# Kernel tuning notes

Hardware: AMD Instinct MI355X
Metric: run time of the kernel (lower is better)

Reference implementation:

```python
import jax, jax.numpy as jnp
import numpy as np

NUM_HEADS = 8
GROUPS = 32
EPS = 1e-5


def setup_inputs() -> dict:
    key = jax.random.key(0)
    k1, k2, k3 = jax.random.split(key, 3)
    B, C, H, W = 16, 512, 64, 64
    x = jax.random.normal(k1, (B, C, H, W), dtype=jnp.float32)
    scale = C ** -0.5  # keep qkv/proj outputs well-scaled
    return {
        "x": x,
        "norm_w": jnp.ones((C,), jnp.float32),
        "norm_b": jnp.zeros((C,), jnp.float32),
        "qkv_w": jax.random.normal(k2, (3 * C, C), dtype=jnp.float32) * scale,
        "qkv_b": jnp.zeros((3 * C,), jnp.float32),
        "proj_w": jax.random.normal(k3, (C, C), dtype=jnp.float32) * scale,
        "proj_b": jnp.zeros((C,), jnp.float32),
    }


def reference(x, norm_w, norm_b, qkv_w, qkv_b, proj_w, proj_b):
    B, C, H, W = x.shape
    N = H * W
    nh = NUM_HEADS
    hd = C // nh

    # GroupNorm(32, C)
    xg = x.reshape(B, GROUPS, C // GROUPS, N)
    mu = xg.mean(axis=(2, 3), keepdims=True)
    var = xg.var(axis=(2, 3), keepdims=True)
    h = ((xg - mu) * jax.lax.rsqrt(var + EPS)).reshape(B, C, N)
    h = h * norm_w[None, :, None] + norm_b[None, :, None]

    h = h.transpose(0, 2, 1)  # [B, N, C]
    qkv = (h @ qkv_w.T + qkv_b).reshape(B, N, 3, nh, hd)
    q, k, v = qkv[:, :, 0], qkv[:, :, 1], qkv[:, :, 2]  # each [B, N, nh, hd]

    # Faithful to source: attention over the HEAD axis at each position
    attn = jnp.einsum('bnhd,bngd->bnhg', q, k) * (hd ** -0.5)  # [B, N, nh, nh]
    attn = jax.nn.softmax(attn, axis=-1)
    o = jnp.einsum('bnhg,bngd->bnhd', attn, v).reshape(B, N, C)

    o = o @ proj_w.T + proj_b  # [B, N, C]
    return x + o.transpose(0, 2, 1).reshape(B, C, H, W)
```

## Files before the change

kernel.cpp:

```cpp
#include <hip/hip_runtime.h>

typedef __attribute__((ext_vector_type(8))) short short8v;
typedef __attribute__((ext_vector_type(4))) float float4v;
typedef unsigned short ushortT;

__device__ __forceinline__ unsigned short f2bf(float f) {
  union { float f; unsigned u; } a; a.f = f;
  unsigned r = a.u + 0x7fffu + ((a.u >> 16) & 1u);
  return (unsigned short)(r >> 16);
}
__device__ __forceinline__ float2 up2(unsigned u) {
  union { unsigned u; float f; } a, b;
  a.u = u << 16; b.u = u & 0xffff0000u;
  return make_float2(a.f, b.f);
}
__device__ __forceinline__ void gl_lds16(const void* g, void* l) {
  __builtin_amdgcn_global_load_lds(
      (const __attribute__((address_space(1))) void*)g,
      (__attribute__((address_space(3))) void*)l, 16, 0, 0);
}

#define WAITV8 asm volatile("s_waitcnt vmcnt(8)" ::: "memory")
#define WAITV4 asm volatile("s_waitcnt vmcnt(4)" ::: "memory")
#define WAITV0 asm volatile("s_waitcnt vmcnt(0)" ::: "memory")
#define BAR()  __builtin_amdgcn_s_barrier()

__global__ __launch_bounds__(256) void wconv(const float* __restrict__ src,
                                             ushortT* __restrict__ dst, int n) {
  int i = (blockIdx.x * 256 + threadIdx.x) * 4;
  if (i < n) {
    float4 v = *(const float4*)(src + i);
    uint2 o;
    o.x = (unsigned)f2bf(v.x) | ((unsigned)f2bf(v.y) << 16);
    o.y = (unsigned)f2bf(v.z) | ((unsigned)f2bf(v.w) << 16);
    *(uint2*)(dst + i) = o;
  }
}

__global__ __launch_bounds__(256) void gn_stats(const float* __restrict__ x,
                                                float2* __restrict__ stats) {
  int bg = blockIdx.x;
  const float* base = x + (size_t)bg * 65536;
  int tid = threadIdx.x;
  float s = 0.f, s2 = 0.f;
  for (int i = tid; i < 16384; i += 256) {
    float4 v = *(const float4*)(base + (size_t)i * 4);
    s  += v.x + v.y + v.z + v.w;
    s2 += v.x * v.x + v.y * v.y + v.z * v.z + v.w * v.w;
  }
  #pragma unroll
  for (int off = 32; off > 0; off >>= 1) {
    s  += __shfl_down(s, off);
    s2 += __shfl_down(s2, off);
  }
  __shared__ float red[8];
  int w = tid >> 6, l = tid & 63;
  if (l == 0) { red[w] = s; red[w + 4] = s2; }
  __syncthreads();
  if (tid == 0) {
    float ts = red[0] + red[1] + red[2] + red[3];
    float t2 = red[4] + red[5] + red[6] + red[7];
    float mean = ts * (1.f / 65536.f);
    float var  = t2 * (1.f / 65536.f) - mean * mean;
    stats[bg] = make_float2(mean, rsqrtf(var + 1e-5f));
  }
}

__global__ __launch_bounds__(512) void norm_tr(const float* __restrict__ x,
                                               const float* __restrict__ nw,
                                               const float* __restrict__ nb,
                                               const float2* __restrict__ stats,
                                               ushortT* __restrict__ h) {
  __shared__ float t[64][65];
  int n0 = blockIdx.x * 64, c0 = blockIdx.y * 64, b = blockIdx.z;
  int tx = threadIdx.x, ty = threadIdx.y;
  #pragma unroll
  for (int j = ty; j < 64; j += 8) {
    int c = c0 + j;
    float2 ms = stats[b * 32 + (c >> 4)];
    float v = x[((size_t)b * 512 + c) * 4096 + n0 + tx];
    t[j][tx] = (v - ms.x) * ms.y * nw[c] + nb[c];
  }
  __syncthreads();
  #pragma unroll
  for (int j = ty; j < 64; j += 8) {
    int n = n0 + j;
    h[((size_t)b * 4096 + n) * 512 + c0 + tx] = f2bf(t[tx][j]);
  }
}

__device__ __forceinline__ void core256(const ushortT* __restrict__ A,
                                        const ushortT* __restrict__ Bm,
                                        ushortT* lds, int m0, int n0,
                                        float4v (&acc)[8][4]) {
  const int tid = threadIdx.x;
  const int w = tid >> 6, l = tid & 63;
  const int wm = w >> 2, wn = w & 3;
  const int ra = w * 32 + (l >> 2);
  const int sc = ((l & 3) ^ ((ra >> 1) & 3)) * 8;
  const ushortT* pa = A + (size_t)(m0 + ra) * 512 + sc;
  const ushortT* pb = Bm + (size_t)(n0 + ra) * 512 + sc;
  const int dstoff = w * 1024;
  const int swz = ((l >> 4) ^ (((l & 15) >> 1) & 3)) * 8;
  const int baseA = (wm * 128 + (l & 15)) * 32 + swz;
  const int baseB = 8192 + (wn * 64 + (l & 15)) * 32 + swz;

  auto stageA = [&](int t) {
    ushortT* d = lds + (t & 3) * 16384 + dstoff;
    gl_lds16(pa + t * 32, d);
    gl_lds16(pa + t * 32 + 16 * 512, d + 512);
  };
  auto stageB = [&](int t) {
    ushortT* d = lds + (t & 3) * 16384 + 8192 + dstoff;
    gl_lds16(pb + t * 32, d);
    gl_lds16(pb + t * 32 + 16 * 512, d + 512);
  };

  stageA(0); stageB(0); stageA(1); stageB(1); stageA(2); stageB(2);
  WAITV8; BAR();

  #pragma unroll 1
  for (int t = 0; t < 16; ++t) {
    const ushortT* buf = lds + (t & 3) * 16384;
    short8v a[8];
    #pragma unroll
    for (int fm = 0; fm < 8; ++fm)
      a[fm] = *(const short8v*)(buf + baseA + fm * 512);
    short8v b0 = *(const short8v*)(buf + baseB);
    short8v b1 = *(const short8v*)(buf + baseB + 512);
    if (t + 3 < 16) stageA(t + 3);
    BAR();
    __builtin_amdgcn_s_setprio(1);
    #pragma unroll
    for (int fm = 0; fm < 8; ++fm) {
      acc[fm][0] = __builtin_amdgcn_mfma_f32_16x16x32_bf16(a[fm], b0, acc[fm][0], 0, 0, 0);
      acc[fm][1] = __builtin_amdgcn_mfma_f32_16x16x32_bf16(a[fm], b1, acc[fm][1], 0, 0, 0);
    }
    __builtin_amdgcn_s_setprio(0);
    BAR();
    short8v b2 = *(const short8v*)(buf + baseB + 1024);
    short8v b3 = *(const short8v*)(buf + baseB + 1536);
    if (t + 3 < 16) stageB(t + 3);
    BAR();
    __builtin_amdgcn_s_setprio(1);
    #pragma unroll
    for (int fm = 0; fm < 8; ++fm) {
      acc[fm][2] = __builtin_amdgcn_mfma_f32_16x16x32_bf16(a[fm], b2, acc[fm][2], 0, 0, 0);
      acc[fm][3] = __builtin_amdgcn_mfma_f32_16x16x32_bf16(a[fm], b3, acc[fm][3], 0, 0, 0);
    }
    __builtin_amdgcn_s_setprio(0);
    if (t <= 12)      { WAITV8; }
    else if (t == 13) { WAITV4; }
    else              { WAITV0; }
    BAR();
  }
}

__global__ __launch_bounds__(512, 2) void gemm_qkv(const ushortT* __restrict__ h,
                                                   const ushortT* __restrict__ wq,
                                                   const float* __restrict__ bias,
                                                   ushortT* __restrict__ outq) {
  __shared__ ushortT lds[65536];
  int bid = blockIdx.x;
  int wg = (bid & 7) * 192 + (bid >> 3);
  int m0 = (wg / 6) * 256, n0 = (wg % 6) * 256;
  float4v acc[8][4] = {};
  core256(h, wq, lds, m0, n0, acc);
  const int tid = threadIdx.x;
  const int w = tid >> 6, l = tid & 63;
  const int wm = w >> 2, wn = w & 3;
  __syncthreads();
  ushortT* es = lds + w * 1280;
  float bb[4];
  #pragma unroll
  for (int fn = 0; fn < 4; ++fn) bb[fn] = bias[n0 + wn * 64 + fn * 16 + (l & 15)];
  int r = l >> 2, g = l & 3;
  #pragma unroll
  for (int fm = 0; fm < 8; ++fm) {
    #pragma unroll
    for (int fn = 0; fn < 4; ++fn)
      #pragma unroll
      for (int j = 0; j < 4; ++j)
        es[((l >> 4) * 4 + j) * 72 + fn * 16 + (l & 15)] = f2bf(acc[fm][fn][j] + bb[fn]);
    uint4 v0 = *(const uint4*)(es + r * 72 + g * 16);
    uint4 v1 = *(const uint4*)(es + r * 72 + g * 16 + 8);
    size_t mrow = (size_t)m0 + wm * 128 + fm * 16 + r;
    uint4* dst = (uint4*)(outq + mrow * 1536 + n0 + wn * 64 + g * 16);
    dst[0] = v0; dst[1] = v1;
  }
}

__global__ __launch_bounds__(256) void attn_k(const ushortT* __restrict__ qkv,
                                              ushortT* __restrict__ o) {
  int gp = blockIdx.x * 256 + threadIdx.x;
  int pos = gp >> 3, hh = gp & 7;
  const ushortT* base = qkv + (size_t)pos * 1536;
  float q[64];
  #pragma unroll
  for (int i = 0; i < 8; ++i) {
    uint4 u = *(const uint4*)(base + hh * 64 + i * 8);
    float2 t0 = up2(u.x), t1 = up2(u.y), t2 = up2(u.z), t3 = up2(u.w);
    q[i*8+0]=t0.x; q[i*8+1]=t0.y; q[i*8+2]=t1.x; q[i*8+3]=t1.y;
    q[i*8+4]=t2.x; q[i*8+5]=t2.y; q[i*8+6]=t3.x; q[i*8+7]=t3.y;
  }
  float lg[8];
  #pragma unroll
  for (int g = 0; g < 8; ++g) {
    float s = 0.f;
    #pragma unroll
    for (int d8 = 0; d8 < 8; ++d8) {
      uint4 kk = *(const uint4*)(base + 512 + g * 64 + d8 * 8);
      float2 k0 = up2(kk.x), k1 = up2(kk.y), k2 = up2(kk.z), k3 = up2(kk.w);
      s += q[d8*8+0]*k0.x + q[d8*8+1]*k0.y + q[d8*8+2]*k1.x + q[d8*8+3]*k1.y
         + q[d8*8+4]*k2.x + q[d8*8+5]*k2.y + q[d8*8+6]*k3.x + q[d8*8+7]*k3.y;
    }
    lg[g] = s * 0.125f;
  }
  float mx = lg[0];
  #pragma unroll
  for (int g = 1; g < 8; ++g) mx = fmaxf(mx, lg[g]);
  float ssum = 0.f;
  #pragma unroll
  for (int g = 0; g < 8; ++g) { lg[g] = __expf(lg[g] - mx); ssum += lg[g]; }
  float inv = 1.f / ssum;
  #pragma unroll
  for (int g = 0; g < 8; ++g) lg[g] *= inv;
  float oa[64];
  #pragma unroll
  for (int i = 0; i < 64; ++i) oa[i] = 0.f;
  #pragma unroll
  for (int g = 0; g < 8; ++g) {
    float wg = lg[g];
    #pragma unroll
    for (int d8 = 0; d8 < 8; ++d8) {
      uint4 vv = *(const uint4*)(base + 1024 + g * 64 + d8 * 8);
      float2 v0 = up2(vv.x), v1 = up2(vv.y), v2 = up2(vv.z), v3 = up2(vv.w);
      oa[d8*8+0] += wg*v0.x; oa[d8*8+1] += wg*v0.y;
      oa[d8*8+2] += wg*v1.x; oa[d8*8+3] += wg*v1.y;
      oa[d8*8+4] += wg*v2.x; oa[d8*8+5] += wg*v2.y;
      oa[d8*8+6] += wg*v3.x; oa[d8*8+7] += wg*v3.y;
    }
  }
  ushortT* dst = o + (size_t)pos * 512 + hh * 64;
  #pragma unroll
  for (int i = 0; i < 8; ++i) {
    uint4 w_;
    w_.x = (unsigned)f2bf(oa[i*8+0]) | ((unsigned)f2bf(oa[i*8+1]) << 16);
    w_.y = (unsigned)f2bf(oa[i*8+2]) | ((unsigned)f2bf(oa[i*8+3]) << 16);
    w_.z = (unsigned)f2bf(oa[i*8+4]) | ((unsigned)f2bf(oa[i*8+5]) << 16);
    w_.w = (unsigned)f2bf(oa[i*8+6]) | ((unsigned)f2bf(oa[i*8+7]) << 16);
    *(uint4*)(dst + i * 8) = w_;
  }
}

__global__ __launch_bounds__(512, 2) void gemm_proj(const ushortT* __restrict__ o,
                                                    const ushortT* __restrict__ wp,
                                                    const float* __restrict__ bias,
                                                    const float* __restrict__ x,
                                                    float* __restrict__ out) {
  __shared__ ushortT lds[65536];
  int bid = blockIdx.x;
  int wg = (bid & 7) * 64 + (bid >> 3);
  int m0 = (wg >> 1) * 256, n0 = (wg & 1) * 256;
  float4v acc[8][4] = {};
  core256(o, wp, lds, m0, n0, acc);
  const int tid = threadIdx.x;
  const int w = tid >> 6, l = tid & 63;
  const int wm = w >> 2, wn = w & 3;
  __syncthreads();
  float* es = (float*)((char*)lds + w * 4608);
  int b = m0 >> 12;
  int c = n0 + wn * 64 + l;
  float bc = bias[c];
  const float* xrow = x + ((size_t)b * 512 + c) * 4096;
  float* orow = out + ((size_t)b * 512 + c) * 4096;
  int nb0 = (m0 & 4095) + wm * 128;
  #pragma unroll
  for (int fm = 0; fm < 8; ++fm) {
    #pragma unroll
    for (int fn = 0; fn < 4; ++fn)
      #pragma unroll
      for (int j = 0; j < 4; ++j)
        es[((l >> 4) * 4 + j) * 68 + fn * 16 + (l & 15)] = acc[fm][fn][j];
    int nb = nb0 + fm * 16;
    #pragma unroll
    for (int q4 = 0; q4 < 4; ++q4) {
      float4 xv = *(const float4*)(xrow + nb + q4 * 4);
      float4 ov;
      ov.x = xv.x + bc + es[(q4 * 4 + 0) * 68 + l];
      ov.y = xv.y + bc + es[(q4 * 4 + 1) * 68 + l];
      ov.z = xv.z + bc + es[(q4 * 4 + 2) * 68 + l];
      ov.w = xv.w + bc + es[(q4 * 4 + 3) * 68 + l];
      *(float4*)(orow + nb + q4 * 4) = ov;
    }
  }
}

extern "C" void kernel_launch(void* const* d_in, const int* in_sizes, int n_in,
                              void* d_out, int out_size, void* d_ws, size_t ws_size,
                              hipStream_t stream) {
  const float* x     = (const float*)d_in[0];
  const float* nw    = (const float*)d_in[1];
  const float* nb    = (const float*)d_in[2];
  const float* qkvw  = (const float*)d_in[3];
  const float* qkvb  = (const float*)d_in[4];
  const float* pw    = (const float*)d_in[5];
  const float* pb    = (const float*)d_in[6];
  float* out = (float*)d_out;
  char* ws = (char*)d_ws;

  const size_t OFF_WQ   = 4096;
  const size_t OFF_WP   = OFF_WQ + 1572864;
  const size_t OFF_H    = OFF_WP + 524288;
  const size_t OFF_QKV  = OFF_H + 67108864;

  float2* stats   = (float2*)ws;
  ushortT* wq_b   = (ushortT*)(ws + OFF_WQ);
  ushortT* wp_b   = (ushortT*)(ws + OFF_WP);
  ushortT* h      = (ushortT*)(ws + OFF_H);
  ushortT* qkv    = (ushortT*)(ws + OFF_QKV);

  wconv<<<768, 256, 0, stream>>>(qkvw, wq_b, 786432);
  wconv<<<256, 256, 0, stream>>>(pw,   wp_b, 262144);
  gn_stats<<<512, 256, 0, stream>>>(x, stats);
  norm_tr<<<dim3(64, 8, 16), dim3(64, 8), 0, stream>>>(x, nw, nb, stats, h);
  gemm_qkv<<<1536, 512, 0, stream>>>(h, wq_b, qkvb, qkv);
  attn_k<<<2048, 256, 0, stream>>>(qkv, h);
  gemm_proj<<<512, 512, 0, stream>>>(h, wp_b, pb, x, out);
}
```

Baseline: 428.0 us.

## Prefetch next K-tile LDS fragments into double-buffered registers during MFMA phases

The GEMM core loop now loads the next tile's A and B fragments from LDS into a second register set, interleaved with the current tile's MFMA phases, using ping-pong register arrays and a loop unrolled by two. Waits are tightened so the next LDS buffer's global loads have completed before those early reads. The aim is to hide LDS read latency behind matrix math. In exchange it roughly doubles the A/B fragment register footprint, which risks spills under the 512-thread, 2-block launch bound, and the changed vmcnt accounting must stay correct.

```diff
diff --git a/kernel.cpp b/kernel.cpp
--- a/kernel.cpp
+++ b/kernel.cpp
@@ -20,10 +20,10 @@
       (__attribute__((address_space(3))) void*)l, 16, 0, 0);
 }
 
-#define WAITV8 asm volatile("s_waitcnt vmcnt(8)" ::: "memory")
 #define WAITV4 asm volatile("s_waitcnt vmcnt(4)" ::: "memory")
 #define WAITV0 asm volatile("s_waitcnt vmcnt(0)" ::: "memory")
 #define BAR()  __builtin_amdgcn_s_barrier()
+#define MFMA16(d, a, b) d = __builtin_amdgcn_mfma_f32_16x16x32_bf16(a, b, d, 0, 0, 0)
 
 __global__ __launch_bounds__(256) void wconv(const float* __restrict__ src,
                                              ushortT* __restrict__ dst, int n) {
@@ -116,43 +116,59 @@
     gl_lds16(pb + t * 32 + 16 * 512, d + 512);
   };
 
+  short8v aX[8], aY[8], b0X, b1X, b0Y, b1Y, bB0, bB1;
+
   stageA(0); stageB(0); stageA(1); stageB(1); stageA(2); stageB(2);
-  WAITV8; BAR();
-
-  #pragma unroll 1
-  for (int t = 0; t < 16; ++t) {
-    const ushortT* buf = lds + (t & 3) * 16384;
-    short8v a[8];
-    #pragma unroll
-    for (int fm = 0; fm < 8; ++fm)
-      a[fm] = *(const short8v*)(buf + baseA + fm * 512);
-    short8v b0 = *(const short8v*)(buf + baseB);
-    short8v b1 = *(const short8v*)(buf + baseB + 512);
+  WAITV4; BAR();
+  #pragma unroll
+  for (int i = 0; i < 8; ++i) aX[i] = *(const short8v*)(lds + baseA + i * 512);
+  b0X = *(const short8v*)(lds + baseB);
+  b1X = *(const short8v*)(lds + baseB + 512);
+
+  auto tile = [&](int t, short8v (&ac)[8], short8v (&an)[8],
+                  short8v& b0c, short8v& b1c, short8v& b0n, short8v& b1n) {
+    const ushortT* buf  = lds + (t & 3) * 16384;
+    const ushortT* bufN = lds + ((t + 1) & 3) * 16384;
+    bB0 = *(const short8v*)(buf + baseB + 1024);
+    bB1 = *(const short8v*)(buf + baseB + 1536);
+    if (t < 15) {
+      #pragma unroll
+      for (int i = 0; i < 4; ++i) an[i] = *(const short8v*)(bufN + baseA + i * 512);
+    }
     if (t + 3 < 16) stageA(t + 3);
     BAR();
     __builtin_amdgcn_s_setprio(1);
     #pragma unroll
     for (int fm = 0; fm < 8; ++fm) {
-      acc[fm][0] = __builtin_amdgcn_mfma_f32_16x16x32_bf16(a[fm], b0, acc[fm][0], 0, 0, 0);
-      acc[fm][1] = __builtin_amdgcn_mfma_f32_16x16x32_bf16(a[fm], b1, acc[fm][1], 0, 0, 0);
+      MFMA16(acc[fm][0], ac[fm], b0c);
+      MFMA16(acc[fm][1], ac[fm], b1c);
     }
     __builtin_amdgcn_s_setprio(0);
     BAR();
-    short8v b2 = *(const short8v*)(buf + baseB + 1024);
-    short8v b3 = *(const short8v*)(buf + baseB + 1536);
+    if (t < 15) {
+      #pragma unroll
+      for (int i = 4; i < 8; ++i) an[i] = *(const short8v*)(bufN + baseA + i * 512);
+      b0n = *(const short8v*)(bufN + baseB);
+      b1n = *(const short8v*)(bufN + baseB + 512);
+    }
     if (t + 3 < 16) stageB(t + 3);
     BAR();
     __builtin_amdgcn_s_setprio(1);
     #pragma unroll
     for (int fm = 0; fm < 8; ++fm) {
-      acc[fm][2] = __builtin_amdgcn_mfma_f32_16x16x32_bf16(a[fm], b2, acc[fm][2], 0, 0, 0);
-      acc[fm][3] = __builtin_amdgcn_mfma_f32_16x16x32_bf16(a[fm], b3, acc[fm][3], 0, 0, 0);
+      MFMA16(acc[fm][2], ac[fm], bB0);
+      MFMA16(acc[fm][3], ac[fm], bB1);
     }
     __builtin_amdgcn_s_setprio(0);
-    if (t <= 12)      { WAITV8; }
-    else if (t == 13) { WAITV4; }
-    else              { WAITV0; }
+    if (t <= 12)      { WAITV4; }
+    else if (t == 13) { WAITV0; }
     BAR();
+  };
+
+  #pragma unroll 1
+  for (int tt = 0; tt < 16; tt += 2) {
+    tile(tt,     aX, aY, b0X, b1X, b0Y, b1Y);
+    tile(tt + 1, aY, aX, b0Y, b1Y, b0X, b1X);
   }
 }
 
```

Measured after the change: 409.2 us. 1.05x faster.

## Restructure GEMM mainloop to K=64 double-buffered tiles with quadrant MFMA clusters

Applied to the files above, without the earlier changes.

Replaces the 4-stage K=32 pipeline in the shared GEMM core with a 2-buffer K=64 scheme. Each K tile is staged as four 128-row half-tiles with an XOR swizzle, and the MFMA work is split into four quadrant clusters, each preceded by fragment reads and interleaved with async global-to-LDS loads for the next tile. The aim is to halve the loop iterations and barrier count per K, and to keep fewer A fragments live at once so register pressure drops. In exchange there are more barriers inside each tile, explicit lgkmcnt waits, and a more fragile ordering of staging writes into the buffer being consumed. The old core256 (also rewritten) is left unused.

```diff
diff --git a/kernel.cpp b/kernel.cpp
--- a/kernel.cpp
+++ b/kernel.cpp
@@ -20,10 +20,11 @@
       (__attribute__((address_space(3))) void*)l, 16, 0, 0);
 }
 
-#define WAITV8 asm volatile("s_waitcnt vmcnt(8)" ::: "memory")
 #define WAITV4 asm volatile("s_waitcnt vmcnt(4)" ::: "memory")
 #define WAITV0 asm volatile("s_waitcnt vmcnt(0)" ::: "memory")
+#define LGKM0  asm volatile("s_waitcnt lgkmcnt(0)" ::: "memory")
 #define BAR()  __builtin_amdgcn_s_barrier()
+#define MFMA16(d, a, b) d = __builtin_amdgcn_mfma_f32_16x16x32_bf16(a, b, d, 0, 0, 0)
 
 __global__ __launch_bounds__(256) void wconv(const float* __restrict__ src,
                                              ushortT* __restrict__ dst, int n) {
@@ -93,67 +94,199 @@
                                         const ushortT* __restrict__ Bm,
                                         ushortT* lds, int m0, int n0,
                                         float4v (&acc)[8][4]) {
+  char* ldsb = (char*)lds;
   const int tid = threadIdx.x;
   const int w = tid >> 6, l = tid & 63;
   const int wm = w >> 2, wn = w & 3;
-  const int ra = w * 32 + (l >> 2);
-  const int sc = ((l & 3) ^ ((ra >> 1) & 3)) * 8;
-  const ushortT* pa = A + (size_t)(m0 + ra) * 512 + sc;
-  const ushortT* pb = Bm + (size_t)(n0 + ra) * 512 + sc;
-  const int dstoff = w * 1024;
-  const int swz = ((l >> 4) ^ (((l & 15) >> 1) & 3)) * 8;
-  const int baseA = (wm * 128 + (l & 15)) * 32 + swz;
-  const int baseB = 8192 + (wn * 64 + (l & 15)) * 32 + swz;
-
-  auto stageA = [&](int t) {
-    ushortT* d = lds + (t & 3) * 16384 + dstoff;
-    gl_lds16(pa + t * 32, d);
-    gl_lds16(pa + t * 32 + 16 * 512, d + 512);
-  };
-  auto stageB = [&](int t) {
-    ushortT* d = lds + (t & 3) * 16384 + 8192 + dstoff;
-    gl_lds16(pb + t * 32, d);
-    gl_lds16(pb + t * 32 + 16 * 512, d + 512);
-  };
-
-  stageA(0); stageB(0); stageA(1); stageB(1); stageA(2); stageB(2);
-  WAITV8; BAR();
+
+  const int P0b = tid * 16, P1b = 8192 + tid * 16;
+  const int r0 = P0b >> 7, r1 = P1b >> 7;
+  const int s0 = (P0b & 127) ^ ((r0 & 7) << 4);
+  const int s1 = (P1b & 127) ^ ((r1 & 7) << 4);
+  const size_t g0 = (size_t)r0 * 512 + (s0 >> 1);
+  const size_t g1 = (size_t)r1 * 512 + (s1 >> 1);
+  auto stage = [&](const ushortT* mat, int rowbase, int kt, int bufb, int region) {
+    const ushortT* gsrc = mat + (size_t)rowbase * 512 + kt * 64;
+    char* dbase = ldsb + bufb + region;
+    gl_lds16(gsrc + g0, dbase + P0b);
+    gl_lds16(gsrc + g1, dbase + P1b);
+  };
+
+  const int colb = (l >> 4) * 16;
+  const int cs0 = colb ^ ((l & 7) << 4);
+  const int cs1 = (64 + colb) ^ ((l & 7) << 4);
+  const int arow = wm * 16384 + (l & 15) * 128;
+  const int brow = 32768 + wn * 8192 + (l & 15) * 128;
+
+  short8v Af[4][2], Bf[4][2];
+  auto rdA = [&](int bb, int m, int mhalf) {
+    const char* p = ldsb + bb + arow + m * 2048;
+    Af[m][0] = *(const short8v*)(p + cs0);
+    Af[m][1] = *(const short8v*)(p + cs1);
+    (void)mhalf;
+  };
+  auto rdB = [&](int bb, int n) {
+    const char* p = ldsb + bb + brow + n * 2048;
+    Bf[n][0] = *(const short8v*)(p + cs0);
+    Bf[n][1] = *(const short8v*)(p + cs1);
+  };
+
+  #define CLUSTER(MH, NP)                                              \
+    { __builtin_amdgcn_s_setprio(1);                                   \
+      _Pragma("unroll")                                                \
+      for (int mm = 0; mm < 4; ++mm) {                                 \
+        _Pragma("unroll")                                              \
+        for (int nn = 0; nn < 2; ++nn) {                               \
+          MFMA16(acc[(MH)*4+mm][(NP)*2+nn], Af[mm][0], Bf[(NP)*2+nn][0]); \
+          MFMA16(acc[(MH)*4+mm][(NP)*2+nn], Af[mm][1], Bf[(NP)*2+nn][1]); \
+        } }                                                            \
+      __builtin_amdgcn_s_setprio(0); }
+
+  auto tile = [&](int bb, int t1, int t2, bool s1g, bool s2g, int vw) {
+    rdA(bb, 0, 0); rdA(bb, 1, 0); rdA(bb, 2, 0); rdA(bb, 3, 0);
+    rdB(bb, 0); rdB(bb, 1);
+    if (s1g) stage(A, m0 + 128, t1, bb ^ 65536, 16384);
+    BAR(); LGKM0;
+    CLUSTER(0, 0);
+    BAR();
+    rdB(bb, 2); rdB(bb, 3);
+    if (s1g) stage(Bm, n0 + 128, t1, bb ^ 65536, 49152);
+    BAR(); LGKM0;
+    CLUSTER(0, 1);
+    BAR();
+    rdA(bb, 0, 1); rdA(bb, 1, 1); rdA(bb, 2, 1); rdA(bb, 3, 1);
+    if (s2g) stage(Bm, n0, t2, bb, 32768);
+    BAR(); LGKM0;
+    CLUSTER(1, 1);
+    BAR();
+    if (s2g) stage(A, m0, t2, bb, 0);
+    if (vw == 4)      { WAITV4; }
+    else if (vw == 0) { WAITV0; }
+    BAR();
+    CLUSTER(1, 0);
+    BAR();
+  };
+  #undef CLUSTER
+
+
+  stage(A,  m0,       0, 0, 0);
+  stage(A,  m0 + 128, 0, 0, 16384);
+  stage(Bm, n0,       0, 0, 32768);
+  stage(Bm, n0 + 128, 0, 0, 49152);
+  stage(Bm, n0,       1, 65536, 32768);
+  stage(A,  m0,       1, 65536, 0);
+  WAITV4;
+  BAR();
 
   #pragma unroll 1
-  for (int t = 0; t < 16; ++t) {
-    const ushortT* buf = lds + (t & 3) * 16384;
-    short8v a[8];
-    #pragma unroll
-    for (int fm = 0; fm < 8; ++fm)
-      a[fm] = *(const short8v*)(buf + baseA + fm * 512);
-    short8v b0 = *(const short8v*)(buf + baseB);
-    short8v b1 = *(const short8v*)(buf + baseB + 512);
-    if (t + 3 < 16) stageA(t + 3);
-    BAR();
-    __builtin_amdgcn_s_setprio(1);
-    #pragma unroll
-    for (int fm = 0; fm < 8; ++fm) {
-      acc[fm][0] = __builtin_amdgcn_mfma_f32_16x16x32_bf16(a[fm], b0, acc[fm][0], 0, 0, 0);
-      acc[fm][1] = __builtin_amdgcn_mfma_f32_16x16x32_bf16(a[fm], b1, acc[fm][1], 0, 0, 0);
-    }
-    __builtin_amdgcn_s_setprio(0);
-    BAR();
-    short8v b2 = *(const short8v*)(buf + baseB + 1024);
-    short8v b3 = *(const short8v*)(buf + baseB + 1536);
-    if (t + 3 < 16) stageB(t + 3);
-    BAR();
-    __builtin_amdgcn_s_setprio(1);
-    #pragma unroll
-    for (int fm = 0; fm < 8; ++fm) {
-      acc[fm][2] = __builtin_amdgcn_mfma_f32_16x16x32_bf16(a[fm], b2, acc[fm][2], 0, 0, 0);
-      acc[fm][3] = __builtin_amdgcn_mfma_f32_16x16x32_bf16(a[fm], b3, acc[fm][3], 0, 0, 0);
-    }
-    __builtin_amdgcn_s_setprio(0);
-    if (t <= 12)      { WAITV8; }
-    else if (t == 13) { WAITV4; }
-    else              { WAITV0; }
-    BAR();
-  }
+  for (int tp = 0; tp < 3; ++tp) {
+    int ta = 2 * tp, tb = 2 * tp + 1;
+    tile(0,     ta + 1, ta + 2, true, true, 4);
+    tile(65536, tb + 1, tb + 2, true, true, 4);
+  }
+  tile(0,     7, 8, true,  false, 0);
+  tile(65536, 8, 9, false, false, -1);
+}
+
+
+__device__ __forceinline__ void core256b(const ushortT* __restrict__ A,
+                                         const ushortT* __restrict__ Bm,
+                                         ushortT* lds, int m0, int n0,
+                                         float4v (&acc)[8][4]) {
+  char* ldsb = (char*)lds;
+  const int tid = threadIdx.x;
+  const int w = tid >> 6, l = tid & 63;
+  const int wm = w >> 2, wn = w & 3;
+
+  const int P0b = tid * 16, P1b = 8192 + tid * 16;
+  const int r0 = P0b >> 7, r1 = P1b >> 7;
+  const int s0 = (P0b & 127) ^ ((r0 & 7) << 4);
+  const int s1 = (P1b & 127) ^ ((r1 & 7) << 4);
+  const size_t g0 = (size_t)r0 * 512 + (s0 >> 1);
+  const size_t g1 = (size_t)r1 * 512 + (s1 >> 1);
+  auto stage = [&](const ushortT* mat, int rowbase, int kt, int bufb, int region) {
+    const ushortT* gsrc = mat + (size_t)rowbase * 512 + kt * 64;
+    char* dbase = ldsb + bufb + region;
+    gl_lds16(gsrc + g0, dbase + P0b);
+    gl_lds16(gsrc + g1, dbase + P1b);
+  };
+
+  const int colb = (l >> 4) * 16;
+  const int cs0 = colb ^ ((l & 7) << 4);
+  const int cs1 = (64 + colb) ^ ((l & 7) << 4);
+  const int arow = wm * 16384 + (l & 15) * 128;
+  const int brow = 32768 + wn * 8192 + (l & 15) * 128;
+
+  short8v Af[4][2], Bf[4][2];
+
+  #define RDA4(bb, MH)                                                  \
+    { _Pragma("unroll")                                                 \
+      for (int mm = 0; mm < 4; ++mm) {                                  \
+        const char* p = ldsb + (bb) + arow + ((MH)*4 + mm) * 2048;      \
+        Af[mm][0] = *(const short8v*)(p + cs0);                         \
+        Af[mm][1] = *(const short8v*)(p + cs1);                         \
+      } }
+  #define RDB2(bb, N0)                                                  \
+    { _Pragma("unroll")                                                 \
+      for (int nn = 0; nn < 2; ++nn) {                                  \
+        const char* p = ldsb + (bb) + brow + ((N0) + nn) * 2048;        \
+        Bf[(N0)+nn][0] = *(const short8v*)(p + cs0);                    \
+        Bf[(N0)+nn][1] = *(const short8v*)(p + cs1);                    \
+      } }
+  #define CLUSTER(MH, NP)                                               \
+    { __builtin_amdgcn_s_setprio(1);                                    \
+      _Pragma("unroll")                                                 \
+      for (int mm = 0; mm < 4; ++mm) {                                  \
+        _Pragma("unroll")                                               \
+        for (int nn = 0; nn < 2; ++nn) {                                \
+          MFMA16(acc[(MH)*4+mm][(NP)*2+nn], Af[mm][0], Bf[(NP)*2+nn][0]); \
+          MFMA16(acc[(MH)*4+mm][(NP)*2+nn], Af[mm][1], Bf[(NP)*2+nn][1]); \
+        } }                                                             \
+      __builtin_amdgcn_s_setprio(0); }
+
+  auto tile = [&](int bb, int t1, int t2, bool s1g, bool s2g, int vw) {
+    RDA4(bb, 0); RDB2(bb, 0);
+    if (s1g) stage(A, m0 + 128, t1, bb ^ 65536, 16384);
+    BAR(); LGKM0;
+    CLUSTER(0, 0);
+    BAR();
+    RDB2(bb, 2);
+    if (s1g) stage(Bm, n0 + 128, t1, bb ^ 65536, 49152);
+    BAR(); LGKM0;
+    CLUSTER(0, 1);
+    BAR();
+    RDA4(bb, 1);
+    if (s2g) stage(Bm, n0, t2, bb, 32768);
+    BAR(); LGKM0;
+    CLUSTER(1, 1);
+    BAR();
+    if (s2g) stage(A, m0, t2, bb, 0);
+    if (vw == 4)      { WAITV4; }
+    else if (vw == 0) { WAITV0; }
+    BAR();
+    CLUSTER(1, 0);
+    BAR();
+  };
+
+  stage(A,  m0,       0, 0, 0);
+  stage(A,  m0 + 128, 0, 0, 16384);
+  stage(Bm, n0,       0, 0, 32768);
+  stage(Bm, n0 + 128, 0, 0, 49152);
+  stage(Bm, n0,       1, 65536, 32768);
+  stage(A,  m0,       1, 65536, 0);
+  WAITV4;
+  BAR();
+
+  #pragma unroll 1
+  for (int tp = 0; tp < 3; ++tp) {
+    tile(0,     2 * tp + 1, 2 * tp + 2, true, true, 4);
+    tile(65536, 2 * tp + 2, 2 * tp + 3, true, true, 4);
+  }
+  tile(0,     7, 8, true,  false, 0);
+  tile(65536, 8, 9, false, false, -1);
+  #undef RDA4
+  #undef RDB2
+  #undef CLUSTER
 }
 
 __global__ __launch_bounds__(512, 2) void gemm_qkv(const ushortT* __restrict__ h,
@@ -165,7 +298,7 @@
   int wg = (bid & 7) * 192 + (bid >> 3);
   int m0 = (wg / 6) * 256, n0 = (wg % 6) * 256;
   float4v acc[8][4] = {};
-  core256(h, wq, lds, m0, n0, acc);
+  core256b(h, wq, lds, m0, n0, acc);
   const int tid = threadIdx.x;
   const int w = tid >> 6, l = tid & 63;
   const int wm = w >> 2, wn = w & 3;
@@ -263,7 +396,7 @@
   int wg = (bid & 7) * 64 + (bid >> 3);
   int m0 = (wg >> 1) * 256, n0 = (wg & 1) * 256;
   float4v acc[8][4] = {};
-  core256(o, wp, lds, m0, n0, acc);
+  core256b(o, wp, lds, m0, n0, acc);
   const int tid = threadIdx.x;
   const int w = tid >> 6, l = tid & 63;
   const int wm = w >> 2, wn = w & 3;
```

Measured after the change: 406.7 us. 1.05x faster.

## Rewrite GEMM core with 32x32x16 MFMA, 64-wide K tiles, persistent N loop

Applied to the files above, without the earlier changes.

Replaces the 16x16x32 MFMA GEMM core with a 32x32x16 version that stages 64-wide K tiles into two swizzled LDS buffers, with global-to-LDS loads interleaved between compute quarters. Each GEMM block now loops over all N tiles for its M strip, which cuts the grid to 256 blocks, fewer than the previous 1536 and 512. The intent is fewer LDS reads per FLOP, fewer barriers and reuse of the A strip across N tiles. The trade-off is lower parallelism: 256 blocks on a chip with 256 CUs, one wave of work and serialized N tiles. The per-tile barrier and wait sequence is also more intricate.

```diff
diff --git a/kernel.cpp b/kernel.cpp
--- a/kernel.cpp
+++ b/kernel.cpp
@@ -1,7 +1,7 @@
 #include <hip/hip_runtime.h>
 
 typedef __attribute__((ext_vector_type(8))) short short8v;
-typedef __attribute__((ext_vector_type(4))) float float4v;
+typedef __attribute__((ext_vector_type(16))) float float16v;
 typedef unsigned short ushortT;
 
 __device__ __forceinline__ unsigned short f2bf(float f) {
@@ -20,10 +20,11 @@
       (__attribute__((address_space(3))) void*)l, 16, 0, 0);
 }
 
-#define WAITV8 asm volatile("s_waitcnt vmcnt(8)" ::: "memory")
 #define WAITV4 asm volatile("s_waitcnt vmcnt(4)" ::: "memory")
 #define WAITV0 asm volatile("s_waitcnt vmcnt(0)" ::: "memory")
+#define LGKM0  asm volatile("s_waitcnt lgkmcnt(0)" ::: "memory")
 #define BAR()  __builtin_amdgcn_s_barrier()
+#define MFMA32(d, a, b) d = __builtin_amdgcn_mfma_f32_32x32x16_bf16(a, b, d, 0, 0, 0)
 
 __global__ __launch_bounds__(256) void wconv(const float* __restrict__ src,
                                              ushortT* __restrict__ dst, int n) {
@@ -89,71 +90,98 @@
   }
 }
 
-__device__ __forceinline__ void core256(const ushortT* __restrict__ A,
-                                        const ushortT* __restrict__ Bm,
-                                        ushortT* lds, int m0, int n0,
-                                        float4v (&acc)[8][4]) {
+__device__ __forceinline__ void core256w(const ushortT* __restrict__ A,
+                                         const ushortT* __restrict__ Bm,
+                                         ushortT* lds, int m0, int n0,
+                                         float16v (&acc)[4][2]) {
+  char* ldsb = (char*)lds;
   const int tid = threadIdx.x;
   const int w = tid >> 6, l = tid & 63;
   const int wm = w >> 2, wn = w & 3;
-  const int ra = w * 32 + (l >> 2);
-  const int sc = ((l & 3) ^ ((ra >> 1) & 3)) * 8;
-  const ushortT* pa = A + (size_t)(m0 + ra) * 512 + sc;
-  const ushortT* pb = Bm + (size_t)(n0 + ra) * 512 + sc;
-  const int dstoff = w * 1024;
-  const int swz = ((l >> 4) ^ (((l & 15) >> 1) & 3)) * 8;
-  const int baseA = (wm * 128 + (l & 15)) * 32 + swz;
-  const int baseB = 8192 + (wn * 64 + (l & 15)) * 32 + swz;
-
-  auto stageA = [&](int t) {
-    ushortT* d = lds + (t & 3) * 16384 + dstoff;
-    gl_lds16(pa + t * 32, d);
-    gl_lds16(pa + t * 32 + 16 * 512, d + 512);
-  };
-  auto stageB = [&](int t) {
-    ushortT* d = lds + (t & 3) * 16384 + 8192 + dstoff;
-    gl_lds16(pb + t * 32, d);
-    gl_lds16(pb + t * 32 + 16 * 512, d + 512);
-  };
-
-  stageA(0); stageB(0); stageA(1); stageB(1); stageA(2); stageB(2);
-  WAITV8; BAR();
+
+  const int P0b = tid * 16, P1b = 8192 + tid * 16;
+  const int r0 = P0b >> 7, r1 = P1b >> 7;
+  const int s0 = (P0b & 127) ^ ((r0 & 7) << 4);
+  const int s1 = (P1b & 127) ^ ((r1 & 7) << 4);
+  const size_t g0 = (size_t)r0 * 512 + (s0 >> 1);
+  const size_t g1 = (size_t)r1 * 512 + (s1 >> 1);
+  auto stage = [&](const ushortT* mat, int rowbase, int kt, int bufb, int region) {
+    const ushortT* gsrc = mat + (size_t)rowbase * 512 + kt * 64;
+    char* dbase = ldsb + bufb + region;
+    gl_lds16(gsrc + g0, dbase + P0b);
+    gl_lds16(gsrc + g1, dbase + P1b);
+  };
+
+  const int rsw   = (l & 7) << 4;
+  const int khalf = (l >> 5) * 16;
+  const int arow = wm * 16384 + (l & 31) * 128;
+  const int brow = 32768 + wn * 8192 + (l & 31) * 128;
+
+  short8v Af[2][4], Bf[2][4];
+  auto rdA = [&](int bb, int mp) {
+    #pragma unroll
+    for (int m2 = 0; m2 < 2; ++m2)
+      #pragma unroll
+      for (int ks = 0; ks < 4; ++ks)
+        Af[m2][ks] = *(const short8v*)(ldsb + bb + arow + (mp * 2 + m2) * 4096
+                                       + ((ks * 32 + khalf) ^ rsw));
+  };
+  auto rdB = [&](int bb, int nn) {
+    #pragma unroll
+    for (int ks = 0; ks < 4; ++ks)
+      Bf[nn][ks] = *(const short8v*)(ldsb + bb + brow + nn * 4096
+                                     + ((ks * 32 + khalf) ^ rsw));
+  };
+  auto cl = [&](int mp, int nn) {
+    __builtin_amdgcn_s_setprio(1);
+    #pragma unroll
+    for (int m2 = 0; m2 < 2; ++m2)
+      #pragma unroll
+      for (int ks = 0; ks < 4; ++ks)
+        MFMA32(acc[mp * 2 + m2][nn], Af[m2][ks], Bf[nn][ks]);
+    __builtin_amdgcn_s_setprio(0);
+  };
+
+  auto tile = [&](int bb, int t1, int t2, bool s1g, bool s2g, int vw) {
+    rdA(bb, 0); rdB(bb, 0);
+    if (s1g) stage(A, m0 + 128, t1, bb ^ 65536, 16384);
+    BAR(); LGKM0;
+    cl(0, 0);
+    BAR();
+    rdB(bb, 1);
+    if (s1g) stage(Bm, n0 + 128, t1, bb ^ 65536, 49152);
+    BAR(); LGKM0;
+    cl(0, 1);
+    BAR();
+    rdA(bb, 1);
+    if (s2g) stage(Bm, n0, t2, bb, 32768);
+    BAR(); LGKM0;
+    cl(1, 1);
+    BAR();
+    if (s2g) stage(A, m0, t2, bb, 0);
+    if (vw == 4)      { WAITV4; }
+    else if (vw == 0) { WAITV0; }
+    BAR();
+    cl(1, 0);
+    BAR();
+  };
+
+  stage(A,  m0,       0, 0, 0);
+  stage(A,  m0 + 128, 0, 0, 16384);
+  stage(Bm, n0,       0, 0, 32768);
+  stage(Bm, n0 + 128, 0, 0, 49152);
+  stage(Bm, n0,       1, 65536, 32768);
+  stage(A,  m0,       1, 65536, 0);
+  WAITV4;
+  BAR();
 
   #pragma unroll 1
-  for (int t = 0; t < 16; ++t) {
-    const ushortT* buf = lds + (t & 3) * 16384;
-    short8v a[8];
-    #pragma unroll
-    for (int fm = 0; fm < 8; ++fm)
-      a[fm] = *(const short8v*)(buf + baseA + fm * 512);
-    short8v b0 = *(const short8v*)(buf + baseB);
-    short8v b1 = *(const short8v*)(buf + baseB + 512);
-    if (t + 3 < 16) stageA(t + 3);
-    BAR();
-    __builtin_amdgcn_s_setprio(1);
-    #pragma unroll
-    for (int fm = 0; fm < 8; ++fm) {
-      acc[fm][0] = __builtin_amdgcn_mfma_f32_16x16x32_bf16(a[fm], b0, acc[fm][0], 0, 0, 0);
-      acc[fm][1] = __builtin_amdgcn_mfma_f32_16x16x32_bf16(a[fm], b1, acc[fm][1], 0, 0, 0);
-    }
-    __builtin_amdgcn_s_setprio(0);
-    BAR();
-    short8v b2 = *(const short8v*)(buf + baseB + 1024);
-    short8v b3 = *(const short8v*)(buf + baseB + 1536);
-    if (t + 3 < 16) stageB(t + 3);
-    BAR();
-    __builtin_amdgcn_s_setprio(1);
-    #pragma unroll
-    for (int fm = 0; fm < 8; ++fm) {
-      acc[fm][2] = __builtin_amdgcn_mfma_f32_16x16x32_bf16(a[fm], b2, acc[fm][2], 0, 0, 0);
-      acc[fm][3] = __builtin_amdgcn_mfma_f32_16x16x32_bf16(a[fm], b3, acc[fm][3], 0, 0, 0);
-    }
-    __builtin_amdgcn_s_setprio(0);
-    if (t <= 12)      { WAITV8; }
-    else if (t == 13) { WAITV4; }
-    else              { WAITV0; }
-    BAR();
-  }
+  for (int tp = 0; tp < 3; ++tp) {
+    tile(0,     2 * tp + 1, 2 * tp + 2, true, true, 4);
+    tile(65536, 2 * tp + 2, 2 * tp + 3, true, true, 4);
+  }
+  tile(0,     7, 8, true,  false, 0);
+  tile(65536, 8, 9, false, false, -1);
 }
 
 __global__ __launch_bounds__(512, 2) void gemm_qkv(const ushortT* __restrict__ h,
@@ -161,32 +189,42 @@
                                                    const float* __restrict__ bias,
                                                    ushortT* __restrict__ outq) {
   __shared__ ushortT lds[65536];
-  int bid = blockIdx.x;
-  int wg = (bid & 7) * 192 + (bid >> 3);
-  int m0 = (wg / 6) * 256, n0 = (wg % 6) * 256;
-  float4v acc[8][4] = {};
-  core256(h, wq, lds, m0, n0, acc);
+  const int m0 = blockIdx.x * 256;
   const int tid = threadIdx.x;
   const int w = tid >> 6, l = tid & 63;
   const int wm = w >> 2, wn = w & 3;
-  __syncthreads();
-  ushortT* es = lds + w * 1280;
-  float bb[4];
-  #pragma unroll
-  for (int fn = 0; fn < 4; ++fn) bb[fn] = bias[n0 + wn * 64 + fn * 16 + (l & 15)];
-  int r = l >> 2, g = l & 3;
-  #pragma unroll
-  for (int fm = 0; fm < 8; ++fm) {
-    #pragma unroll
-    for (int fn = 0; fn < 4; ++fn)
-      #pragma unroll
-      for (int j = 0; j < 4; ++j)
-        es[((l >> 4) * 4 + j) * 72 + fn * 16 + (l & 15)] = f2bf(acc[fm][fn][j] + bb[fn]);
-    uint4 v0 = *(const uint4*)(es + r * 72 + g * 16);
-    uint4 v1 = *(const uint4*)(es + r * 72 + g * 16 + 8);
-    size_t mrow = (size_t)m0 + wm * 128 + fm * 16 + r;
-    uint4* dst = (uint4*)(outq + mrow * 1536 + n0 + wn * 64 + g * 16);
-    dst[0] = v0; dst[1] = v1;
+  const int lcol = l & 31, lhi = l >> 5;
+
+  #pragma unroll 1
+  for (int ni = 0; ni < 6; ++ni) {
+    const int n0 = ni * 256;
+    float16v acc[4][2] = {};
+    core256w(h, wq, lds, m0, n0, acc);
+    __syncthreads();
+    ushortT* es = lds + w * 2304;
+    float bb2[2];
+    #pragma unroll
+    for (int nn = 0; nn < 2; ++nn) bb2[nn] = bias[n0 + wn * 64 + nn * 32 + lcol];
+    const int row2 = l >> 1, g = l & 1;
+    #pragma unroll
+    for (int mm = 0; mm < 4; ++mm) {
+      #pragma unroll
+      for (int nn = 0; nn < 2; ++nn)
+        #pragma unroll
+        for (int r = 0; r < 16; ++r) {
+          int row = (r & 3) + 8 * (r >> 2) + 4 * lhi;
+          es[row * 72 + nn * 32 + lcol] = f2bf(acc[mm][nn][r] + bb2[nn]);
+        }
+      const ushortT* ep = es + row2 * 72 + g * 32;
+      uint4 v0 = *(const uint4*)(ep);
+      uint4 v1 = *(const uint4*)(ep + 8);
+      uint4 v2 = *(const uint4*)(ep + 16);
+      uint4 v3 = *(const uint4*)(ep + 24);
+      size_t mrow = (size_t)m0 + wm * 128 + mm * 32 + row2;
+      uint4* dst = (uint4*)(outq + mrow * 1536 + n0 + wn * 64 + g * 32);
+      dst[0] = v0; dst[1] = v1; dst[2] = v2; dst[3] = v3;
+    }
+    __syncthreads();
   }
 }
 
@@ -259,40 +297,49 @@
                                                     const float* __restrict__ x,
                                                     float* __restrict__ out) {
   __shared__ ushortT lds[65536];
-  int bid = blockIdx.x;
-  int wg = (bid & 7) * 64 + (bid >> 3);
-  int m0 = (wg >> 1) * 256, n0 = (wg & 1) * 256;
-  float4v acc[8][4] = {};
-  core256(o, wp, lds, m0, n0, acc);
+  const int m0 = blockIdx.x * 256;
   const int tid = threadIdx.x;
   const int w = tid >> 6, l = tid & 63;
   const int wm = w >> 2, wn = w & 3;
-  __syncthreads();
-  float* es = (float*)((char*)lds + w * 4608);
-  int b = m0 >> 12;
-  int c = n0 + wn * 64 + l;
-  float bc = bias[c];
-  const float* xrow = x + ((size_t)b * 512 + c) * 4096;
-  float* orow = out + ((size_t)b * 512 + c) * 4096;
-  int nb0 = (m0 & 4095) + wm * 128;
-  #pragma unroll
-  for (int fm = 0; fm < 8; ++fm) {
-    #pragma unroll
-    for (int fn = 0; fn < 4; ++fn)
-      #pragma unroll
-      for (int j = 0; j < 4; ++j)
-        es[((l >> 4) * 4 + j) * 68 + fn * 16 + (l & 15)] = acc[fm][fn][j];
-    int nb = nb0 + fm * 16;
-    #pragma unroll
-    for (int q4 = 0; q4 < 4; ++q4) {
-      float4 xv = *(const float4*)(xrow + nb + q4 * 4);
-      float4 ov;
-      ov.x = xv.x + bc + es[(q4 * 4 + 0) * 68 + l];
-      ov.y = xv.y + bc + es[(q4 * 4 + 1) * 68 + l];
-      ov.z = xv.z + bc + es[(q4 * 4 + 2) * 68 + l];
-      ov.w = xv.w + bc + es[(q4 * 4 + 3) * 68 + l];
-      *(float4*)(orow + nb + q4 * 4) = ov;
+  const int lcol = l & 31, lhi = l >> 5;
+  const int b = m0 >> 12;
+  const int nb0 = (m0 & 4095) + wm * 128;
+
+  #pragma unroll 1
+  for (int ni = 0; ni < 2; ++ni) {
+    const int n0 = ni * 256;
+    float16v acc[4][2] = {};
+    core256w(o, wp, lds, m0, n0, acc);
+    __syncthreads();
+    float* esf = (float*)((char*)lds + w * 9216);
+    const int c = n0 + wn * 64 + l;
+    const float bc = bias[c];
+    const float* xrow = x + ((size_t)b * 512 + c) * 4096;
+    float* orow = out + ((size_t)b * 512 + c) * 4096;
+    #pragma unroll
+    for (int mm = 0; mm < 4; ++mm) {
+      #pragma unroll
+      for (int nn = 0; nn < 2; ++nn)
+        #pragma unroll
+        for (int r = 0; r < 16; ++r) {
+          int pos = (r & 3) + 8 * (r >> 2) + 4 * lhi;
+          esf[(nn * 32 + lcol) * 36 + pos] = acc[mm][nn][r];
+        }
+      int nb = nb0 + mm * 32;
+      #pragma unroll
+      for (int pg = 0; pg < 8; ++pg) {
+        float4 xv = *(const float4*)(xrow + nb + pg * 4);
+        float4 ev = *(const float4*)(esf + l * 36 + pg * 4);
+        float4 ov;
+        ov.x = xv.x + bc + ev.x;
+        ov.y = xv.y + bc + ev.y;
+        ov.z = xv.z + bc + ev.z;
+        ov.w = xv.w + bc + ev.w;
+        *(float4*)(orow + nb + pg * 4) = ov;
+      }
+      __syncthreads();
     }
+    __syncthreads();
   }
 }
 
@@ -324,7 +371,7 @@
   wconv<<<256, 256, 0, stream>>>(pw,   wp_b, 262144);
   gn_stats<<<512, 256, 0, stream>>>(x, stats);
   norm_tr<<<dim3(64, 8, 16), dim3(64, 8), 0, stream>>>(x, nw, nb, stats, h);
-  gemm_qkv<<<1536, 512, 0, stream>>>(h, wq_b, qkvb, qkv);
+  gemm_qkv<<<256, 512, 0, stream>>>(h, wq_b, qkvb, qkv);
   attn_k<<<2048, 256, 0, stream>>>(qkv, h);
-  gemm_proj<<<512, 512, 0, stream>>>(h, wp_b, pb, x, out);
-}
+  gemm_proj<<<256, 512, 0, stream>>>(h, wp_b, pb, x, out);
+}
```

Result: slower. 462.5 us (+8.1%).
